# Kernel optimization log

Measured on AMD Instinct MI355X. Metric: run time of the kernel, lower is better.

## Reference

```python
import jax, jax.numpy as jnp
import numpy as np

D_MODEL = 1024
N_HEADS = 16
D_K = D_MODEL // N_HEADS
SCALE = float(np.sqrt(D_K))


def setup_inputs() -> dict:
    key = jax.random.key(0)
    ks = jax.random.split(key, 8)
    B, S = 2, 2048
    std = 1.0 / np.sqrt(D_MODEL)
    return {
        "query": jax.random.normal(ks[0], (B, S, D_MODEL), dtype=jnp.float32),
        "key": jax.random.normal(ks[1], (B, S, D_MODEL), dtype=jnp.float32),
        "value": jax.random.normal(ks[2], (B, S, D_MODEL), dtype=jnp.float32),
        "w_q": jax.random.normal(ks[3], (D_MODEL, D_MODEL), dtype=jnp.float32) * std,
        "w_k": jax.random.normal(ks[4], (D_MODEL, D_MODEL), dtype=jnp.float32) * std,
        "w_v": jax.random.normal(ks[5], (D_MODEL, D_MODEL), dtype=jnp.float32) * std,
        "w_o": jax.random.normal(ks[6], (D_MODEL, D_MODEL), dtype=jnp.float32) * std,
        "b_o": jax.random.normal(ks[7], (D_MODEL,), dtype=jnp.float32) * std,
    }


def reference(query, key, value, w_q, w_k, w_v, w_o, b_o):
    B, S, _ = query.shape
    # torch nn.Linear: y = x @ W^T
    def proj(x, w):
        # [B,S,D] -> [B,H,S,d_k]
        y = jnp.einsum("bsd,ed->bse", x, w)
        return y.reshape(B, S, N_HEADS, D_K).transpose(0, 2, 1, 3)

    Q = proj(query, w_q)
    K = proj(key, w_k)
    V = proj(value, w_v)
    scores = jnp.einsum("bhqd,bhkd->bhqk", Q, K) / SCALE  # [B,H,S,S]
    attn = jax.nn.softmax(scores, axis=-1)
    # dropout is identity in eval mode
    ctx = jnp.einsum("bhqk,bhkd->bhqd", attn, V)  # [B,H,S,d_k]
    ctx = ctx.transpose(0, 2, 1, 3).reshape(B, S, D_MODEL)
    out = jnp.einsum("bsd,ed->bse", ctx, w_o) + b_o
    return out, attn
```

## Files before the change

### kernel.cpp

```cpp
#include <hip/hip_runtime.h>
#include <cstdint>
#include <cstddef>

#define SEQ   2048
#define NH    16
#define DKD   64
#define DM    1024

typedef __attribute__((ext_vector_type(8))) short bf16x8;
typedef __attribute__((ext_vector_type(4))) short bf16x4;
typedef __attribute__((ext_vector_type(4))) float f32x4;
typedef unsigned short u16;

__device__ __forceinline__ u16 f2bf(float f) {
    union { float f; unsigned u; } v; v.f = f;
    unsigned r = v.u + 0x7fff + ((v.u >> 16) & 1);
    return (u16)(r >> 16);
}
__device__ __forceinline__ float bf2f(u16 b) {
    union { unsigned u; float f; } v; v.u = ((unsigned)b) << 16;
    return v.f;
}

__device__ __forceinline__ void gload16(const void* g, void* l) {
    __builtin_amdgcn_global_load_lds(
        (const __attribute__((address_space(1))) void*)g,
        (__attribute__((address_space(3))) void*)l, 16, 0, 0);
}

__global__ __launch_bounds__(256)
void cast_all(const float* __restrict__ q, const float* __restrict__ k,
              const float* __restrict__ v, const float* __restrict__ wq,
              const float* __restrict__ wk, const float* __restrict__ wv,
              const float* __restrict__ wo,
              u16* __restrict__ qb, u16* __restrict__ kb, u16* __restrict__ vb,
              u16* __restrict__ wb) {
    const int z = blockIdx.y;
    const float* s;
    u16* d;
    if (z < 12) {
        int a = z >> 2;
        s = (a == 0 ? q : a == 1 ? k : v) + (size_t)(z & 3) * 1048576;
        d = (a == 0 ? qb : a == 1 ? kb : vb) + (size_t)(z & 3) * 1048576;
    } else {
        int a = z - 12;
        s = (a == 0 ? wq : a == 1 ? wk : a == 2 ? wv : wo);
        d = wb + (size_t)a * 1048576;
    }
    size_t i = ((size_t)blockIdx.x * 256 + threadIdx.x) * 8;
    f32x4 x0 = *(const f32x4*)&s[i];
    f32x4 x1 = *(const f32x4*)&s[i + 4];
    bf16x8 o;
#pragma unroll
    for (int j = 0; j < 4; j++) { o[j] = (short)f2bf(x0[j]); o[j + 4] = (short)f2bf(x1[j]); }
    *(bf16x8*)&d[i] = o;
}

__global__ __launch_bounds__(256, 3)
void qkv_gemm(const u16* __restrict__ qb, const u16* __restrict__ kb,
              const u16* __restrict__ vb, const u16* __restrict__ wb,
              u16* __restrict__ Qw, u16* __restrict__ Kw, u16* __restrict__ Vtw) {
    __shared__ u16 As[128][64];
    __shared__ u16 Bs[128][64];

    const int z = blockIdx.z;
    const u16* A  = (z == 0) ? qb : (z == 1) ? kb : vb;
    const u16* Bm = wb + (size_t)z * 1048576;
    u16*      dst = (z == 0) ? Qw : (z == 1) ? Kw : Vtw;
    const float sc = (z == 0) ? 0.125f : 1.0f;

    const int t    = threadIdx.x;
    const int m0   = blockIdx.y * 128;
    const int n0   = blockIdx.x * 128;
    const int w    = t >> 6;
    const int ln   = t & 63;
    const int l16  = ln & 15;
    const int quad = ln >> 4;
    const int wr   = (w >> 1) * 64;
    const int wc   = (w & 1) * 64;

    const int sr = ln >> 3;
    const int sc8 = (ln & 7) * 8;

    f32x4 acc[4][4];
#pragma unroll
    for (int i = 0; i < 4; i++)
#pragma unroll
        for (int j = 0; j < 4; j++) {
            f32x4 zz = {0.f, 0.f, 0.f, 0.f};
            acc[i][j] = zz;
        }

    for (int k0 = 0; k0 < 1024; k0 += 64) {
#pragma unroll
        for (int i = 0; i < 4; i++) {
            int chunk = w * 4 + i;
            int r = chunk * 8 + sr;
            gload16(&A [(size_t)(m0 + r) * 1024 + k0 + sc8], &As[chunk * 8][0]);
            gload16(&Bm[(size_t)(n0 + r) * 1024 + k0 + sc8], &Bs[chunk * 8][0]);
        }
        __syncthreads();
#pragma unroll
        for (int ks = 0; ks < 2; ks++) {
            bf16x8 af[4], bfr[4];
#pragma unroll
            for (int i = 0; i < 4; i++)
                af[i] = *(const bf16x8*)&As[wr + i * 16 + l16][ks * 32 + quad * 8];
#pragma unroll
            for (int j = 0; j < 4; j++)
                bfr[j] = *(const bf16x8*)&Bs[wc + j * 16 + l16][ks * 32 + quad * 8];
#pragma unroll
            for (int i = 0; i < 4; i++)
#pragma unroll
                for (int j = 0; j < 4; j++)
                    acc[i][j] = __builtin_amdgcn_mfma_f32_16x16x32_bf16(
                        af[i], bfr[j], acc[i][j], 0, 0, 0);
        }
        __syncthreads();
    }

#pragma unroll
    for (int i = 0; i < 4; i++)
#pragma unroll
        for (int j = 0; j < 4; j++)
#pragma unroll
            for (int r = 0; r < 4; r++) {
                int row = m0 + wr + i * 16 + quad * 4 + r;
                int col = n0 + wc + j * 16 + l16;
                float val = acc[i][j][r] * sc;
                int b = row >> 11, s = row & 2047, h = col >> 6, dk = col & 63;
                if (z < 2)
                    dst[((size_t)((b * 16 + h) * 2048 + s)) * 64 + dk] = f2bf(val);
                else
                    dst[((size_t)((b * 16 + h) * 64 + dk)) * 2048 + s] = f2bf(val);
            }
}

__global__ __launch_bounds__(256, 3)
void out_gemm(const u16* __restrict__ A, const u16* __restrict__ Bm,
              float* __restrict__ dst, const float* __restrict__ bias) {
    __shared__ u16 As[128][64];
    __shared__ u16 Bs[128][64];

    const int t    = threadIdx.x;
    const int m0   = blockIdx.y * 128;
    const int n0   = blockIdx.x * 128;
    const int w    = t >> 6;
    const int ln   = t & 63;
    const int l16  = ln & 15;
    const int quad = ln >> 4;
    const int wr   = (w >> 1) * 64;
    const int wc   = (w & 1) * 64;
    const int sr   = ln >> 3;
    const int sc8  = (ln & 7) * 8;

    f32x4 acc[4][4];
#pragma unroll
    for (int i = 0; i < 4; i++)
#pragma unroll
        for (int j = 0; j < 4; j++) {
            f32x4 zz = {0.f, 0.f, 0.f, 0.f};
            acc[i][j] = zz;
        }

    for (int k0 = 0; k0 < 1024; k0 += 64) {
#pragma unroll
        for (int i = 0; i < 4; i++) {
            int chunk = w * 4 + i;
            int r = chunk * 8 + sr;
            gload16(&A [(size_t)(m0 + r) * 1024 + k0 + sc8], &As[chunk * 8][0]);
            gload16(&Bm[(size_t)(n0 + r) * 1024 + k0 + sc8], &Bs[chunk * 8][0]);
        }
        __syncthreads();
#pragma unroll
        for (int ks = 0; ks < 2; ks++) {
            bf16x8 af[4], bfr[4];
#pragma unroll
            for (int i = 0; i < 4; i++)
                af[i] = *(const bf16x8*)&As[wr + i * 16 + l16][ks * 32 + quad * 8];
#pragma unroll
            for (int j = 0; j < 4; j++)
                bfr[j] = *(const bf16x8*)&Bs[wc + j * 16 + l16][ks * 32 + quad * 8];
#pragma unroll
            for (int i = 0; i < 4; i++)
#pragma unroll
                for (int j = 0; j < 4; j++)
                    acc[i][j] = __builtin_amdgcn_mfma_f32_16x16x32_bf16(
                        af[i], bfr[j], acc[i][j], 0, 0, 0);
        }
        __syncthreads();
    }

#pragma unroll
    for (int i = 0; i < 4; i++)
#pragma unroll
        for (int j = 0; j < 4; j++)
#pragma unroll
            for (int r = 0; r < 4; r++) {
                int row = m0 + wr + i * 16 + quad * 4 + r;
                int col = n0 + wc + j * 16 + l16;
                dst[(size_t)row * 1024 + col] = acc[i][j][r] + bias[col];
            }
}

__global__ __launch_bounds__(256, 3)
void attn_kernel(const u16* __restrict__ Qw, const u16* __restrict__ Kw,
                 const u16* __restrict__ Vtw,
                 float* __restrict__ attn_out, u16* __restrict__ ctx_out) {
    __shared__ u16 Qs[64][72];
    __shared__ u16 KVs[128][72];
    __shared__ u16 Ps[64][136];
    u16 (*Vts)[136] = (u16(*)[136])&KVs[0][0];

    const int t    = threadIdx.x;
    const int bh   = blockIdx.y;
    const int q0   = blockIdx.x * 64;
    const int w    = t >> 6;
    const int lane = t & 63;
    const int l16  = lane & 15;
    const int quad = lane >> 4;

    const u16* Qh = Qw  + (size_t)bh * SEQ * DKD;
    const u16* Kh = Kw  + (size_t)bh * SEQ * DKD;
    const u16* Vh = Vtw + (size_t)bh * DKD * SEQ;

#pragma unroll
    for (int i = 0; i < 2; i++) {
        int c  = t + 256 * i;
        int r  = c >> 3;
        int c8 = (c & 7) * 8;
        *(bf16x8*)&Qs[r][c8] = *(const bf16x8*)&Qh[(size_t)(q0 + r) * 64 + c8];
    }

    float lsum[4];
#pragma unroll
    for (int r = 0; r < 4; r++) lsum[r] = 0.f;

    for (int kt = 0; kt < 16; kt++) {
        __syncthreads();
#pragma unroll
        for (int i = 0; i < 4; i++) {
            int c  = t + 256 * i;
            int r  = c >> 3;
            int c8 = (c & 7) * 8;
            *(bf16x8*)&KVs[r][c8] = *(const bf16x8*)&Kh[(size_t)(kt * 128 + r) * 64 + c8];
        }
        __syncthreads();

        f32x4 s[8];
#pragma unroll
        for (int j = 0; j < 8; j++) { f32x4 zz = {0.f,0.f,0.f,0.f}; s[j] = zz; }
#pragma unroll
        for (int ks = 0; ks < 2; ks++) {
            bf16x8 a = *(const bf16x8*)&Qs[w * 16 + l16][ks * 32 + quad * 8];
#pragma unroll
            for (int j = 0; j < 8; j++) {
                bf16x8 b = *(const bf16x8*)&KVs[j * 16 + l16][ks * 32 + quad * 8];
                s[j] = __builtin_amdgcn_mfma_f32_16x16x32_bf16(a, b, s[j], 0, 0, 0);
            }
        }
#pragma unroll
        for (int j = 0; j < 8; j++)
#pragma unroll
            for (int r = 0; r < 4; r++)
                lsum[r] += __expf(s[j][r]);
    }

    float lnl[4];
#pragma unroll
    for (int r = 0; r < 4; r++) {
#pragma unroll
        for (int d = 1; d < 16; d <<= 1) lsum[r] += __shfl_xor(lsum[r], d, 64);
        lnl[r] = __logf(lsum[r]);
    }

    f32x4 o[4];
#pragma unroll
    for (int jo = 0; jo < 4; jo++) { f32x4 zz = {0.f,0.f,0.f,0.f}; o[jo] = zz; }

    for (int kt = 0; kt < 16; kt++) {
        __syncthreads();
#pragma unroll
        for (int i = 0; i < 4; i++) {
            int c  = t + 256 * i;
            int r  = c >> 3;
            int c8 = (c & 7) * 8;
            *(bf16x8*)&KVs[r][c8] = *(const bf16x8*)&Kh[(size_t)(kt * 128 + r) * 64 + c8];
        }
        __syncthreads();

        f32x4 s[8];
#pragma unroll
        for (int j = 0; j < 8; j++) { f32x4 zz = {0.f,0.f,0.f,0.f}; s[j] = zz; }
#pragma unroll
        for (int ks = 0; ks < 2; ks++) {
            bf16x8 a = *(const bf16x8*)&Qs[w * 16 + l16][ks * 32 + quad * 8];
#pragma unroll
            for (int j = 0; j < 8; j++) {
                bf16x8 b = *(const bf16x8*)&KVs[j * 16 + l16][ks * 32 + quad * 8];
                s[j] = __builtin_amdgcn_mfma_f32_16x16x32_bf16(a, b, s[j], 0, 0, 0);
            }
        }
        __syncthreads();

#pragma unroll
        for (int j = 0; j < 8; j++)
#pragma unroll
            for (int r = 0; r < 4; r++) {
                float p = __expf(s[j][r] - lnl[r]);
                Ps[w * 16 + quad * 4 + r][j * 16 + l16] = f2bf(p);
            }
#pragma unroll
        for (int i = 0; i < 4; i++) {
            int c  = t + 256 * i;
            int r  = c >> 4;
            int c8 = (c & 15) * 8;
            *(bf16x8*)&Vts[r][c8] = *(const bf16x8*)&Vh[(size_t)r * 2048 + kt * 128 + c8];
        }
        __syncthreads();

#pragma unroll
        for (int i = 0; i < 8; i++) {
            int c  = t + 256 * i;
            int r  = c >> 5;
            int c4 = (c & 31) * 4;
            bf16x4 pv = *(const bf16x4*)&Ps[r][c4];
            f32x4 o4;
#pragma unroll
            for (int j = 0; j < 4; j++) o4[j] = bf2f((u16)pv[j]);
            *(f32x4*)&attn_out[((size_t)(bh * 2048 + q0 + r)) * 2048 + kt * 128 + c4] = o4;
        }

        bf16x8 pa[4];
#pragma unroll
        for (int ks = 0; ks < 4; ks++)
            pa[ks] = *(const bf16x8*)&Ps[w * 16 + l16][ks * 32 + quad * 8];
#pragma unroll
        for (int jo = 0; jo < 4; jo++)
#pragma unroll
            for (int ks = 0; ks < 4; ks++) {
                bf16x8 vb = *(const bf16x8*)&Vts[jo * 16 + l16][ks * 32 + quad * 8];
                o[jo] = __builtin_amdgcn_mfma_f32_16x16x32_bf16(pa[ks], vb, o[jo], 0, 0, 0);
            }
    }

    const int b = bh >> 4, h = bh & 15;
#pragma unroll
    for (int jo = 0; jo < 4; jo++)
#pragma unroll
        for (int r = 0; r < 4; r++) {
            int srow = q0 + w * 16 + quad * 4 + r;
            int dcol = h * 64 + jo * 16 + l16;
            ctx_out[((size_t)(b * 2048 + srow)) * 1024 + dcol] = f2bf(o[jo][r]);
        }
}

extern "C" void kernel_launch(void* const* d_in, const int* in_sizes, int n_in,
                              void* d_out, int out_size, void* d_ws, size_t ws_size,
                              hipStream_t stream) {
    (void)in_sizes; (void)n_in; (void)out_size; (void)ws_size;

    const float* q  = (const float*)d_in[0];
    const float* k  = (const float*)d_in[1];
    const float* v  = (const float*)d_in[2];
    const float* wq = (const float*)d_in[3];
    const float* wk = (const float*)d_in[4];
    const float* wv = (const float*)d_in[5];
    const float* wo = (const float*)d_in[6];
    const float* bo = (const float*)d_in[7];

    float* out  = (float*)d_out;
    float* attn = out + (size_t)4194304;

    u16* Qw   = (u16*)d_ws;
    u16* Kw   = Qw   + (size_t)4194304;
    u16* Vtw  = Kw   + (size_t)4194304;
    u16* ctxb = Vtw  + (size_t)4194304;
    u16* qb   = ctxb + (size_t)4194304;
    u16* kb   = qb   + (size_t)4194304;
    u16* vb   = kb   + (size_t)4194304;
    u16* wb   = vb   + (size_t)4194304;

    dim3 blk(256);
    cast_all<<<dim3(512, 16), blk, 0, stream>>>(q, k, v, wq, wk, wv, wo,
                                                qb, kb, vb, wb);
    qkv_gemm<<<dim3(8, 32, 3), blk, 0, stream>>>(qb, kb, vb, wb, Qw, Kw, Vtw);
    attn_kernel<<<dim3(32, 32), blk, 0, stream>>>(Qw, Kw, Vtw, attn, ctxb);
    out_gemm<<<dim3(8, 32), blk, 0, stream>>>(ctxb, wb + (size_t)3 * 1048576, out, bo);
}
```

Baseline: 823.7 us.

## Restructure attention with 512-thread blocks, register prefetch, and XCD-aware block remapping

The attention kernel now uses 512-thread blocks covering 128 query rows and keeps Q fragments in registers instead of shared memory. It prefetches the next K/V tile into registers while the current tile is computed, and double-buffers K in the first pass to remove a barrier. All three GEMM/attention kernels remap block IDs so consecutive blocks on the same XCD share operand tiles for better L2 locality. The larger block and extra prefetch registers may reduce occupancy.

```diff
diff --git a/kernel.cpp b/kernel.cpp
--- a/kernel.cpp
+++ b/kernel.cpp
@@ -63,24 +63,26 @@
     __shared__ u16 As[128][64];
     __shared__ u16 Bs[128][64];
 
-    const int z = blockIdx.z;
+    const int hwid = blockIdx.x + 8 * blockIdx.y + 256 * blockIdx.z;
+    const int lgc  = (hwid & 7) * 96 + (hwid >> 3);
+    const int z    = lgc >> 8;
+    const int m0   = ((lgc >> 3) & 31) * 128;
+    const int n0   = (lgc & 7) * 128;
+
     const u16* A  = (z == 0) ? qb : (z == 1) ? kb : vb;
     const u16* Bm = wb + (size_t)z * 1048576;
     u16*      dst = (z == 0) ? Qw : (z == 1) ? Kw : Vtw;
     const float sc = (z == 0) ? 0.125f : 1.0f;
 
     const int t    = threadIdx.x;
-    const int m0   = blockIdx.y * 128;
-    const int n0   = blockIdx.x * 128;
     const int w    = t >> 6;
     const int ln   = t & 63;
     const int l16  = ln & 15;
     const int quad = ln >> 4;
     const int wr   = (w >> 1) * 64;
     const int wc   = (w & 1) * 64;
-
-    const int sr = ln >> 3;
-    const int sc8 = (ln & 7) * 8;
+    const int sr   = ln >> 3;
+    const int sc8  = (ln & 7) * 8;
 
     f32x4 acc[4][4];
 #pragma unroll
@@ -142,9 +144,12 @@
     __shared__ u16 As[128][64];
     __shared__ u16 Bs[128][64];
 
+    const int hwid = blockIdx.x + 8 * blockIdx.y;
+    const int lgc  = (hwid & 7) * 32 + (hwid >> 3);
+    const int m0   = (lgc >> 3) * 128;
+    const int n0   = (lgc & 7) * 128;
+
     const int t    = threadIdx.x;
-    const int m0   = blockIdx.y * 128;
-    const int n0   = blockIdx.x * 128;
     const int w    = t >> 6;
     const int ln   = t & 63;
     const int l16  = ln & 15;
@@ -203,18 +208,19 @@
             }
 }
 
-__global__ __launch_bounds__(256, 3)
+__global__ __launch_bounds__(512, 4)
 void attn_kernel(const u16* __restrict__ Qw, const u16* __restrict__ Kw,
                  const u16* __restrict__ Vtw,
                  float* __restrict__ attn_out, u16* __restrict__ ctx_out) {
-    __shared__ u16 Qs[64][72];
-    __shared__ u16 KVs[128][72];
-    __shared__ u16 Ps[64][136];
-    u16 (*Vts)[136] = (u16(*)[136])&KVs[0][0];
+    __shared__ u16 H[2][128][72];
+    __shared__ u16 Ps[128][136];
+    u16 (*Vts)[136] = (u16(*)[136])&H[1][0][0];
 
     const int t    = threadIdx.x;
-    const int bh   = blockIdx.y;
-    const int q0   = blockIdx.x * 64;
+    const int hwid = blockIdx.x + 16 * blockIdx.y;
+    const int lgc  = (hwid & 7) * 64 + (hwid >> 3);
+    const int bh   = lgc >> 4;
+    const int q0   = (lgc & 15) * 128;
     const int w    = t >> 6;
     const int lane = t & 63;
     const int l16  = lane & 15;
@@ -224,26 +230,29 @@
     const u16* Kh = Kw  + (size_t)bh * SEQ * DKD;
     const u16* Vh = Vtw + (size_t)bh * DKD * SEQ;
 
-#pragma unroll
-    for (int i = 0; i < 2; i++) {
-        int c  = t + 256 * i;
-        int r  = c >> 3;
-        int c8 = (c & 7) * 8;
-        *(bf16x8*)&Qs[r][c8] = *(const bf16x8*)&Qh[(size_t)(q0 + r) * 64 + c8];
-    }
+    bf16x8 qf[2];
+#pragma unroll
+    for (int ks = 0; ks < 2; ks++)
+        qf[ks] = *(const bf16x8*)&Qh[(size_t)(q0 + w * 16 + l16) * 64 + ks * 32 + quad * 8];
+
+    const int kr0 = t >> 3,         kc0 = (t & 7) * 8;
+    const int kr1 = (t + 512) >> 3, kc1 = ((t + 512) & 7) * 8;
+    const int vr0 = t >> 4,         vc0 = (t & 15) * 8;
+    const int vr1 = (t + 512) >> 4, vc1 = ((t + 512) & 15) * 8;
 
     float lsum[4];
 #pragma unroll
     for (int r = 0; r < 4; r++) lsum[r] = 0.f;
 
+    bf16x8 kp0 = *(const bf16x8*)&Kh[(size_t)kr0 * 64 + kc0];
+    bf16x8 kp1 = *(const bf16x8*)&Kh[(size_t)kr1 * 64 + kc1];
     for (int kt = 0; kt < 16; kt++) {
-        __syncthreads();
-#pragma unroll
-        for (int i = 0; i < 4; i++) {
-            int c  = t + 256 * i;
-            int r  = c >> 3;
-            int c8 = (c & 7) * 8;
-            *(bf16x8*)&KVs[r][c8] = *(const bf16x8*)&Kh[(size_t)(kt * 128 + r) * 64 + c8];
+        u16 (*KA)[72] = H[kt & 1];
+        *(bf16x8*)&KA[kr0][kc0] = kp0;
+        *(bf16x8*)&KA[kr1][kc1] = kp1;
+        if (kt < 15) {
+            kp0 = *(const bf16x8*)&Kh[(size_t)((kt + 1) * 128 + kr0) * 64 + kc0];
+            kp1 = *(const bf16x8*)&Kh[(size_t)((kt + 1) * 128 + kr1) * 64 + kc1];
         }
         __syncthreads();
 
@@ -251,14 +260,12 @@
 #pragma unroll
         for (int j = 0; j < 8; j++) { f32x4 zz = {0.f,0.f,0.f,0.f}; s[j] = zz; }
 #pragma unroll
-        for (int ks = 0; ks < 2; ks++) {
-            bf16x8 a = *(const bf16x8*)&Qs[w * 16 + l16][ks * 32 + quad * 8];
+        for (int ks = 0; ks < 2; ks++)
 #pragma unroll
             for (int j = 0; j < 8; j++) {
-                bf16x8 b = *(const bf16x8*)&KVs[j * 16 + l16][ks * 32 + quad * 8];
-                s[j] = __builtin_amdgcn_mfma_f32_16x16x32_bf16(a, b, s[j], 0, 0, 0);
-            }
-        }
+                bf16x8 b = *(const bf16x8*)&KA[j * 16 + l16][ks * 32 + quad * 8];
+                s[j] = __builtin_amdgcn_mfma_f32_16x16x32_bf16(qf[ks], b, s[j], 0, 0, 0);
+            }
 #pragma unroll
         for (int j = 0; j < 8; j++)
 #pragma unroll
@@ -278,14 +285,21 @@
 #pragma unroll
     for (int jo = 0; jo < 4; jo++) { f32x4 zz = {0.f,0.f,0.f,0.f}; o[jo] = zz; }
 
+    kp0 = *(const bf16x8*)&Kh[(size_t)kr0 * 64 + kc0];
+    kp1 = *(const bf16x8*)&Kh[(size_t)kr1 * 64 + kc1];
+    bf16x8 vp0 = *(const bf16x8*)&Vh[(size_t)vr0 * 2048 + vc0];
+    bf16x8 vp1 = *(const bf16x8*)&Vh[(size_t)vr1 * 2048 + vc1];
     for (int kt = 0; kt < 16; kt++) {
         __syncthreads();
-#pragma unroll
-        for (int i = 0; i < 4; i++) {
-            int c  = t + 256 * i;
-            int r  = c >> 3;
-            int c8 = (c & 7) * 8;
-            *(bf16x8*)&KVs[r][c8] = *(const bf16x8*)&Kh[(size_t)(kt * 128 + r) * 64 + c8];
+        *(bf16x8*)&H[0][kr0][kc0] = kp0;
+        *(bf16x8*)&H[0][kr1][kc1] = kp1;
+        *(bf16x8*)&Vts[vr0][vc0]  = vp0;
+        *(bf16x8*)&Vts[vr1][vc1]  = vp1;
+        if (kt < 15) {
+            kp0 = *(const bf16x8*)&Kh[(size_t)((kt + 1) * 128 + kr0) * 64 + kc0];
+            kp1 = *(const bf16x8*)&Kh[(size_t)((kt + 1) * 128 + kr1) * 64 + kc1];
+            vp0 = *(const bf16x8*)&Vh[(size_t)vr0 * 2048 + (kt + 1) * 128 + vc0];
+            vp1 = *(const bf16x8*)&Vh[(size_t)vr1 * 2048 + (kt + 1) * 128 + vc1];
         }
         __syncthreads();
 
@@ -293,16 +307,12 @@
 #pragma unroll
         for (int j = 0; j < 8; j++) { f32x4 zz = {0.f,0.f,0.f,0.f}; s[j] = zz; }
 #pragma unroll
-        for (int ks = 0; ks < 2; ks++) {
-            bf16x8 a = *(const bf16x8*)&Qs[w * 16 + l16][ks * 32 + quad * 8];
+        for (int ks = 0; ks < 2; ks++)
 #pragma unroll
             for (int j = 0; j < 8; j++) {
-                bf16x8 b = *(const bf16x8*)&KVs[j * 16 + l16][ks * 32 + quad * 8];
-                s[j] = __builtin_amdgcn_mfma_f32_16x16x32_bf16(a, b, s[j], 0, 0, 0);
-            }
-        }
-        __syncthreads();
-
+                bf16x8 b = *(const bf16x8*)&H[0][j * 16 + l16][ks * 32 + quad * 8];
+                s[j] = __builtin_amdgcn_mfma_f32_16x16x32_bf16(qf[ks], b, s[j], 0, 0, 0);
+            }
 #pragma unroll
         for (int j = 0; j < 8; j++)
 #pragma unroll
@@ -310,18 +320,11 @@
                 float p = __expf(s[j][r] - lnl[r]);
                 Ps[w * 16 + quad * 4 + r][j * 16 + l16] = f2bf(p);
             }
-#pragma unroll
-        for (int i = 0; i < 4; i++) {
-            int c  = t + 256 * i;
-            int r  = c >> 4;
-            int c8 = (c & 15) * 8;
-            *(bf16x8*)&Vts[r][c8] = *(const bf16x8*)&Vh[(size_t)r * 2048 + kt * 128 + c8];
-        }
         __syncthreads();
 
 #pragma unroll
         for (int i = 0; i < 8; i++) {
-            int c  = t + 256 * i;
+            int c  = t + 512 * i;
             int r  = c >> 5;
             int c4 = (c & 31) * 4;
             bf16x4 pv = *(const bf16x4*)&Ps[r][c4];
@@ -385,6 +388,6 @@
     cast_all<<<dim3(512, 16), blk, 0, stream>>>(q, k, v, wq, wk, wv, wo,
                                                 qb, kb, vb, wb);
     qkv_gemm<<<dim3(8, 32, 3), blk, 0, stream>>>(qb, kb, vb, wb, Qw, Kw, Vtw);
-    attn_kernel<<<dim3(32, 32), blk, 0, stream>>>(Qw, Kw, Vtw, attn, ctxb);
+    attn_kernel<<<dim3(16, 32), dim3(512), 0, stream>>>(Qw, Kw, Vtw, attn, ctxb);
     out_gemm<<<dim3(8, 32), blk, 0, stream>>>(ctxb, wb + (size_t)3 * 1048576, out, bo);
 }
```

Measured after the change: 712.9 us. 13.5% less time.
